# Optimization experiments

Measured on AMD Instinct MI355X. Metric: run time of the kernel, lower is better.

Reference implementation:

```python
import jax, jax.numpy as jnp
import numpy as np

DIM = 1024
N_HEADS = 16
DIM_FF = 4096
EPS = 1e-12


def layer_norm(x, gamma, beta):
    u = jnp.mean(x, axis=-1, keepdims=True)
    s = jnp.mean((x - u) ** 2, axis=-1, keepdims=True)
    return gamma * ((x - u) / jnp.sqrt(s + EPS)) + beta


def setup_inputs() -> dict:
    key = jax.random.key(0)
    ks = jax.random.split(key, 12)
    B, S, D, F = 2, 2048, DIM, DIM_FF
    init = lambda k, shape: (jax.random.normal(k, shape, dtype=jnp.float32) * 0.02)
    return {
        "x": jax.random.normal(ks[0], (B, S, D), dtype=jnp.float32),
        "mask": jnp.ones((B, S), dtype=jnp.int32),
        "wq": init(ks[1], (D, D)), "bq": jnp.zeros((D,), jnp.float32),
        "wk": init(ks[2], (D, D)), "bk": jnp.zeros((D,), jnp.float32),
        "wv": init(ks[3], (D, D)), "bv": jnp.zeros((D,), jnp.float32),
        "wo": init(ks[4], (D, D)), "bo": jnp.zeros((D,), jnp.float32),
        "g1": jnp.ones((D,), jnp.float32), "b1": jnp.zeros((D,), jnp.float32),
        "w1": init(ks[5], (D, F)), "bf1": jnp.zeros((F,), jnp.float32),
        "w2": init(ks[6], (F, D)), "bf2": jnp.zeros((D,), jnp.float32),
        "g2": jnp.ones((D,), jnp.float32), "b2": jnp.zeros((D,), jnp.float32),
    }


def reference(x, mask, wq, bq, wk, bk, wv, bv, wo, bo, g1, b1, w1, bf1, w2, bf2, g2, b2):
    B, S, D = x.shape
    H = N_HEADS
    W = D // H
    # QKV projections -> (B, H, S, W)
    def heads(y):
        return y.reshape(B, S, H, W).transpose(0, 2, 1, 3)
    q = heads(x @ wq + bq)
    k = heads(x @ wk + bk)
    v = heads(x @ wv + bv)
    # scaled dot-product attention with additive mask (exact module math)
    scores = jnp.einsum('bhsw,bhtw->bhst', q, k) / np.sqrt(W).astype(np.float32)
    m = mask.astype(jnp.float32)[:, None, None, :]  # (B,1,1,S)
    scores = scores - 10000.0 * (1.0 - m)
    attn = jax.nn.softmax(scores, axis=-1)
    h = jnp.einsum('bhst,bhtw->bhsw', attn, v).transpose(0, 2, 1, 3).reshape(B, S, D)
    # residual + LN1
    h = layer_norm(x + (h @ wo + bo), g1, b1)
    # position-wise FFN with exact-erf GELU, residual + LN2
    ff = jax.nn.gelu(h @ w1 + bf1, approximate=False) @ w2 + bf2
    return layer_norm(h + ff, g2, b2)
```

## Files before the change

kernel.cpp:

```cpp
#include <hip/hip_runtime.h>
#include <cstdint>
#include <cstddef>

using u16 = unsigned short;
using u32 = unsigned int;
using u64 = unsigned long long;

typedef __bf16 bf16x8 __attribute__((ext_vector_type(8)));
typedef float f32x4 __attribute__((ext_vector_type(4)));

static constexpr int Bb = 2, S = 2048, D = 1024, H = 16, W = 64, F = 4096;
static constexpr int M = Bb * S;

__device__ __forceinline__ float bf2f(u16 u) {
  union { u32 i; float f; } c; c.i = ((u32)u) << 16; return c.f;
}
__device__ __forceinline__ u16 f2bf(float f) {
  union { float f; u32 i; } c; c.f = f;
  u32 i = c.i;
  u32 r = (i + 0x7fffu + ((i >> 16) & 1u)) >> 16;
  return (u16)r;
}
__device__ __forceinline__ u16 f2bf_cvt(float f) {
  __bf16 b = (__bf16)f;
  union { __bf16 b; u16 u; } c; c.b = b; return c.u;
}
__device__ __forceinline__ __bf16 u2b(u16 x) {
  union { u16 u; __bf16 b; } c; c.u = x; return c.b;
}
__device__ __forceinline__ void stv(float* p, size_t i, float v) { p[i] = v; }
__device__ __forceinline__ void stv(u16* p, size_t i, float v)   { p[i] = f2bf(v); }
__device__ __forceinline__ float ldv(const float* p, size_t i) { return p[i]; }
__device__ __forceinline__ float ldv(const u16* p, size_t i)   { return bf2f(p[i]); }

__device__ __forceinline__ void async_cp16(const u16* g, u16* l) {
  __builtin_amdgcn_global_load_lds(
      (const __attribute__((address_space(1))) void*)g,
      (__attribute__((address_space(3))) void*)l, 16, 0, 0);
}

__device__ __forceinline__ void swizzle8(int& bx, int& by) {
  int bid = blockIdx.y * gridDim.x + blockIdx.x;
  int gpr = gridDim.x >> 3;
  int grp = bid >> 6, rem = bid & 63;
  int gm = grp / gpr, gn = grp - gm * gpr;
  by = gm * 8 + (rem >> 3);
  bx = gn * 8 + (rem & 7);
}

__global__ __launch_bounds__(256) void conv_x_kernel(
    const float* __restrict__ src, u16* __restrict__ dst)
{
  int i = (blockIdx.x * 256 + threadIdx.x) * 4;
  float4 v = *(const float4*)(src + i);
  u16 r[4] = { f2bf(v.x), f2bf(v.y), f2bf(v.z), f2bf(v.w) };
  *(uint2*)(dst + i) = *(const uint2*)r;
}

__global__ __launch_bounds__(256) void transpose_w_kernel(
    const float* __restrict__ src, u16* __restrict__ dst, int K, int N)
{
  __shared__ __align__(16) u16 T[64][72];
  const int tid = threadIdx.x;
  const int n0 = blockIdx.x * 64, k0 = blockIdx.y * 64;
#pragma unroll
  for (int t = 0; t < 4; t++) {
    int idx = tid + t * 256;
    int r = idx >> 4, c4 = (idx & 15) * 4;
    float4 v = *(const float4*)(src + (size_t)(k0 + r) * N + n0 + c4);
    T[c4 + 0][r] = f2bf(v.x); T[c4 + 1][r] = f2bf(v.y);
    T[c4 + 2][r] = f2bf(v.z); T[c4 + 3][r] = f2bf(v.w);
  }
  __syncthreads();
#pragma unroll
  for (int t = 0; t < 2; t++) {
    int idx = tid + t * 256;
    int r = idx >> 3, c8 = (idx & 7) * 8;
    *(uint4*)(dst + (size_t)(n0 + r) * K + k0 + c8) = *(const uint4*)(&T[r][c8]);
  }
}

template<int EPI, typename TC>
__global__ __launch_bounds__(256) void gemm_bt(
    const u16* __restrict__ A, const u16* __restrict__ BT,
    const float* __restrict__ bias, TC* __restrict__ C,
    int N, int K, float scale)
{
  __shared__ __align__(16) u16 As[2][128 * 32];
  __shared__ __align__(16) u16 Bs[2][128 * 32];
  const int tid = threadIdx.x;
  const int wave = tid >> 6, lane = tid & 63;
  const int quad = lane >> 4, l16 = lane & 15;
  int bx, by; swizzle8(bx, by);
  const int m0 = by * 128, n0 = bx * 128;
  const int wm = (wave >> 1) * 64, wn = (wave & 1) * 64;
  const int srow = lane >> 2;
  const int skoff = (lane & 3) * 8;

  f32x4 acc[4][4] = {};

  for (int k0 = 0; k0 < K; k0 += 64) {
#pragma unroll
    for (int h = 0; h < 2; h++) {
#pragma unroll
      for (int t = 0; t < 2; t++) {
        int slot = wave * 2 + t;
        int row = slot * 16 + srow;
        const u16* ga = A  + (size_t)(m0 + row) * K + k0 + h * 32 + skoff;
        const u16* gb = BT + (size_t)(n0 + row) * K + k0 + h * 32 + skoff;
        async_cp16(ga, As[h] + slot * 512);
        async_cp16(gb, Bs[h] + slot * 512);
      }
    }
    __syncthreads();

#pragma unroll
    for (int h = 0; h < 2; h++) {
      bf16x8 af[4], bfv[4];
#pragma unroll
      for (int i = 0; i < 4; i++)
        af[i] = *(const bf16x8*)(As[h] + (wm + i * 16 + l16) * 32 + quad * 8);
#pragma unroll
      for (int j = 0; j < 4; j++)
        bfv[j] = *(const bf16x8*)(Bs[h] + (wn + j * 16 + l16) * 32 + quad * 8);
#pragma unroll
      for (int i = 0; i < 4; i++)
#pragma unroll
        for (int j = 0; j < 4; j++)
          acc[i][j] = __builtin_amdgcn_mfma_f32_16x16x32_bf16(af[i], bfv[j], acc[i][j], 0, 0, 0);
    }
    __syncthreads();
  }

#pragma unroll
  for (int i = 0; i < 4; i++) {
#pragma unroll
    for (int j = 0; j < 4; j++) {
#pragma unroll
      for (int r = 0; r < 4; r++) {
        int row = m0 + wm + i * 16 + quad * 4 + r;
        int col = n0 + wn + j * 16 + l16;
        float val = acc[i][j][r] + bias[col];
        if (EPI == 2) {
          int sel = col >> 10, c = col & 1023;
          if (sel == 0) val *= scale;
          int bb = row >> 11, ss = row & 2047;
          int hh = c >> 6,  ww = c & 63;
          u16* dst = (u16*)C + (size_t)sel * M * D;
          dst[(((size_t)(bb * H + hh) * S) + ss) * W + ww] = f2bf(val);
        } else {
          stv(C, (size_t)row * N + col, val);
        }
      }
    }
  }
}

__global__ __launch_bounds__(512, 2) void gemm256_gelu(
    const u16* __restrict__ A, const u16* __restrict__ BT,
    const float* __restrict__ bias, u16* __restrict__ C)
{
  constexpr int GN = F, GK = D, NT = GK / 64;
  __shared__ __align__(16) u16 AL[2][2][128 * 64];
  __shared__ __align__(16) u16 BL[2][2][128 * 64];
  const int tid = threadIdx.x;
  const int wave = tid >> 6, lane = tid & 63;
  const int quad = lane >> 4, l16 = lane & 15;
  const int wm = wave >> 2, wn = wave & 3;
  int bx, by; swizzle8(bx, by);
  const int m0 = by * 256, n0 = bx * 256;
  const int lr = lane >> 3;
  const int kc8 = ((lane & 7) ^ lr) * 8;
  const int xb = (l16 & 7) * 16;
  const int brow0 = (wn & 1) * 64;
  const char* abase = (const char*)&AL[0][wm][0];
  const char* bbase = (const char*)&BL[0][wn >> 1][0];
  constexpr int BUFB = 2 * 128 * 64 * 2;

  f32x4 acc[8][4] = {};

  auto stA = [&](int t, int buf) {
#pragma unroll
    for (int half = 0; half < 2; half++)
#pragma unroll
      for (int j = 0; j < 2; j++) {
        const u16* g = A + (size_t)(m0 + half * 128 + (j * 8 + wave) * 8 + lr) * GK
                         + t * 64 + kc8;
        async_cp16(g, &AL[buf][half][(j * 8 + wave) * 512]);
      }
  };
  auto stB = [&](int t, int buf, int half) {
#pragma unroll
    for (int j = 0; j < 2; j++) {
      const u16* g = BT + (size_t)(n0 + half * 128 + (j * 8 + wave) * 8 + lr) * GK
                        + t * 64 + kc8;
      async_cp16(g, &BL[buf][half][(j * 8 + wave) * 512]);
    }
  };

  stA(0, 0);
  stB(0, 0, 0); stB(0, 0, 1);
  stB(1, 1, 0); stB(1, 1, 1);
  asm volatile("s_waitcnt vmcnt(4)" ::: "memory");
  __builtin_amdgcn_s_barrier();

  bf16x8 af[4][2], bf0[2][2], bf1v[2][2];

#pragma unroll 2
  for (int t = 0; t < NT; t++) {
    const int buf = t & 1;
    const char* ab = abase + buf * BUFB;
    const char* bb = bbase + buf * BUFB;

#pragma unroll
    for (int i = 0; i < 4; i++)
#pragma unroll
      for (int s = 0; s < 2; s++)
        af[i][s] = *(const bf16x8*)(ab + (i * 16 + l16) * 128 + (((s * 4 + quad) * 16) ^ xb));
#pragma unroll
    for (int j = 0; j < 2; j++)
#pragma unroll
      for (int s = 0; s < 2; s++)
        bf0[j][s] = *(const bf16x8*)(bb + (brow0 + j * 16 + l16) * 128 + (((s * 4 + quad) * 16) ^ xb));
    stA((t + 1) & (NT - 1), buf ^ 1);
    __builtin_amdgcn_s_barrier();
    __builtin_amdgcn_s_setprio(1);
#pragma unroll
    for (int i = 0; i < 4; i++)
#pragma unroll
      for (int j = 0; j < 2; j++)
#pragma unroll
        for (int s = 0; s < 2; s++)
          acc[i][j] = __builtin_amdgcn_mfma_f32_16x16x32_bf16(af[i][s], bf0[j][s], acc[i][j], 0, 0, 0);
    __builtin_amdgcn_s_setprio(0);
    __builtin_amdgcn_s_barrier();

#pragma unroll
    for (int j = 0; j < 2; j++)
#pragma unroll
      for (int s = 0; s < 2; s++)
        bf1v[j][s] = *(const bf16x8*)(bb + (brow0 + 32 + j * 16 + l16) * 128 + (((s * 4 + quad) * 16) ^ xb));
    __builtin_amdgcn_s_barrier();
    __builtin_amdgcn_s_setprio(1);
#pragma unroll
    for (int i = 0; i < 4; i++)
#pragma unroll
      for (int j = 0; j < 2; j++)
#pragma unroll
        for (int s = 0; s < 2; s++)
          acc[i][2 + j] = __builtin_amdgcn_mfma_f32_16x16x32_bf16(af[i][s], bf1v[j][s], acc[i][2 + j], 0, 0, 0);
    __builtin_amdgcn_s_setprio(0);
    __builtin_amdgcn_s_barrier();

#pragma unroll
    for (int i = 0; i < 4; i++)
#pragma unroll
      for (int s = 0; s < 2; s++)
        af[i][s] = *(const bf16x8*)(ab + (64 + i * 16 + l16) * 128 + (((s * 4 + quad) * 16) ^ xb));
    stB((t + 2) & (NT - 1), buf, 0);
    __builtin_amdgcn_s_barrier();
    __builtin_amdgcn_s_setprio(1);
#pragma unroll
    for (int i = 0; i < 4; i++)
#pragma unroll
      for (int j = 0; j < 2; j++)
#pragma unroll
        for (int s = 0; s < 2; s++)
          acc[4 + i][2 + j] = __builtin_amdgcn_mfma_f32_16x16x32_bf16(af[i][s], bf1v[j][s], acc[4 + i][2 + j], 0, 0, 0);
    __builtin_amdgcn_s_setprio(0);
    __builtin_amdgcn_s_barrier();

    stB((t + 2) & (NT - 1), buf, 1);
    __builtin_amdgcn_s_barrier();
    __builtin_amdgcn_s_setprio(1);
#pragma unroll
    for (int i = 0; i < 4; i++)
#pragma unroll
      for (int j = 0; j < 2; j++)
#pragma unroll
        for (int s = 0; s < 2; s++)
          acc[4 + i][j] = __builtin_amdgcn_mfma_f32_16x16x32_bf16(af[i][s], bf0[j][s], acc[4 + i][j], 0, 0, 0);
    __builtin_amdgcn_s_setprio(0);
    asm volatile("s_waitcnt vmcnt(4)" ::: "memory");
    __builtin_amdgcn_s_barrier();
  }

  asm volatile("s_waitcnt vmcnt(0)" ::: "memory");

#pragma unroll
  for (int i = 0; i < 8; i++) {
#pragma unroll
    for (int j = 0; j < 4; j++) {
#pragma unroll
      for (int r = 0; r < 4; r++) {
        int row = m0 + wm * 128 + i * 16 + quad * 4 + r;
        int col = n0 + wn * 64 + j * 16 + l16;
        float val = acc[i][j][r] + bias[col];
        val = 0.5f * val * (1.0f + erff(val * 0.70710678118654752f));
        C[(size_t)row * GN + col] = f2bf(val);
      }
    }
  }
}

template<typename TC>
__global__ __launch_bounds__(256) void gemm_bt_n64(
    const u16* __restrict__ A, const u16* __restrict__ BT,
    const float* __restrict__ bias, TC* __restrict__ C,
    int N, int K)
{
  __shared__ __align__(16) u16 As[2][128 * 32];
  __shared__ __align__(16) u16 Bs[2][64 * 32];
  const int tid = threadIdx.x;
  const int wave = tid >> 6, lane = tid & 63;
  const int quad = lane >> 4, l16 = lane & 15;
  int bx, by; swizzle8(bx, by);
  const int m0 = by * 128, n0 = bx * 64;
  const int wm = (wave >> 1) * 64, wn = (wave & 1) * 32;
  const int srow = lane >> 2;
  const int skoff = (lane & 3) * 8;

  f32x4 acc[4][2] = {};

  for (int k0 = 0; k0 < K; k0 += 64) {
#pragma unroll
    for (int h = 0; h < 2; h++) {
#pragma unroll
      for (int t = 0; t < 2; t++) {
        int slot = wave * 2 + t;
        int row = slot * 16 + srow;
        async_cp16(A + (size_t)(m0 + row) * K + k0 + h * 32 + skoff, As[h] + slot * 512);
      }
      int row = wave * 16 + srow;
      async_cp16(BT + (size_t)(n0 + row) * K + k0 + h * 32 + skoff, Bs[h] + wave * 512);
    }
    __syncthreads();

#pragma unroll
    for (int h = 0; h < 2; h++) {
      bf16x8 af[4], bfv[2];
#pragma unroll
      for (int i = 0; i < 4; i++)
        af[i] = *(const bf16x8*)(As[h] + (wm + i * 16 + l16) * 32 + quad * 8);
#pragma unroll
      for (int j = 0; j < 2; j++)
        bfv[j] = *(const bf16x8*)(Bs[h] + (wn + j * 16 + l16) * 32 + quad * 8);
#pragma unroll
      for (int i = 0; i < 4; i++)
#pragma unroll
        for (int j = 0; j < 2; j++)
          acc[i][j] = __builtin_amdgcn_mfma_f32_16x16x32_bf16(af[i], bfv[j], acc[i][j], 0, 0, 0);
    }
    __syncthreads();
  }

#pragma unroll
  for (int i = 0; i < 4; i++) {
#pragma unroll
    for (int j = 0; j < 2; j++) {
#pragma unroll
      for (int r = 0; r < 4; r++) {
        int row = m0 + wm + i * 16 + quad * 4 + r;
        int col = n0 + wn + j * 16 + l16;
        stv(C, (size_t)row * N + col, acc[i][j][r] + bias[col]);
      }
    }
  }
}

__global__ __launch_bounds__(256) void transpose_v_kernel(
    const u16* __restrict__ v, u16* __restrict__ vt)
{
  __shared__ __align__(16) u16 T[64][72];
  const int bh = blockIdx.y, k0 = blockIdx.x * 64, tid = threadIdx.x;
#pragma unroll
  for (int it = 0; it < 2; it++) {
    int vv = tid + it * 256;
    int key = vv >> 3, w0 = (vv & 7) * 8;
    union { uint4 q; u16 e[8]; } u;
    u.q = *(const uint4*)(v + ((size_t)bh * S + k0 + key) * W + w0);
#pragma unroll
    for (int j = 0; j < 8; j++) T[w0 + j][key] = u.e[j];
  }
  __syncthreads();
#pragma unroll
  for (int it = 0; it < 2; it++) {
    int vv = tid + it * 256;
    int w = vv >> 3, koff = (vv & 7) * 8;
    *(uint4*)(vt + ((size_t)bh * W + w) * S + k0 + koff) = *(const uint4*)(&T[w][koff]);
  }
}

__global__ __launch_bounds__(256) void fattn_kernel(
    const u16* __restrict__ q, const u16* __restrict__ k,
    const u16* __restrict__ vt, const int* __restrict__ mask,
    u16* __restrict__ o_parts, float* __restrict__ l_parts)
{
  __shared__ __align__(16) u16 QP[2][128][32];
  __shared__ __align__(16) u16 Kl[2][64][32];
  __shared__ __align__(16) u16 Vl[2][64][32];

  const int tid = threadIdx.x, wave = tid >> 6, lane = tid & 63;
  const int quad = lane >> 4, l16 = lane & 15;
  const int bh = blockIdx.y, b = bh >> 4, h = bh & 15;
  const int q0 = blockIdx.x * 128;
  const int half = blockIdx.z;
  const int kbase = half * (S / 2);
  const int wq0 = wave * 32;
  const int sr  = tid >> 3;
  const int sg  = tid & 7;
  const int sp  = sg >> 2;
  const int sc0 = sg * 8;
  const int ssw = (((sg & 3) ^ ((sr >> 1) & 3)) << 3);
  const int xr = (l16 >> 1) & 3;
  const int rq = ((quad ^ xr) << 3);

#pragma unroll
  for (int t = 0; t < 4; t++) {
    int row = sr + t * 32;
    *(uint4*)(&QP[sp][row][ssw]) =
        *(const uint4*)(q + ((size_t)bh * S + q0 + row) * W + sc0);
  }
  __syncthreads();
  bf16x8 aq[2][2];
#pragma unroll
  for (int g = 0; g < 2; g++)
#pragma unroll
    for (int kc = 0; kc < 2; kc++)
      aq[g][kc] = *(const bf16x8*)(&QP[kc][wq0 + g * 16 + l16][rq]);

  bf16x8 ones;
  {
    u16 ov = (l16 == 0) ? (u16)0x3F80 : (u16)0;
#pragma unroll
    for (int j = 0; j < 8; j++) ones[j] = u2b(ov);
  }

  f32x4 o_acc[2][4] = {};
  f32x4 l_acc[2] = {};

  uint4 kr0, kr1, vr0, vr1;
  int mv;
  kr0 = *(const uint4*)(k  + ((size_t)bh * S + kbase + sr     ) * W + sc0);
  kr1 = *(const uint4*)(k  + ((size_t)bh * S + kbase + sr + 32) * W + sc0);
  vr0 = *(const uint4*)(vt + ((size_t)bh * W + sr     ) * S + kbase + sc0);
  vr1 = *(const uint4*)(vt + ((size_t)bh * W + sr + 32) * S + kbase + sc0);
  mv  = mask[b * S + kbase + lane];

  constexpr int NT = S / 128;
  for (int kt = 0; kt < NT; kt++) {
    __syncthreads();
    *(uint4*)(&Kl[sp][sr     ][ssw]) = kr0;
    *(uint4*)(&Kl[sp][sr + 32][ssw]) = kr1;
    *(uint4*)(&Vl[sp][sr     ][ssw]) = vr0;
    *(uint4*)(&Vl[sp][sr + 32][ssw]) = vr1;
    u64 km = __ballot(mv != 0);
    __syncthreads();

    if (kt + 1 < NT) {
      int kn = kbase + (kt + 1) * 64;
      kr0 = *(const uint4*)(k  + ((size_t)bh * S + kn + sr     ) * W + sc0);
      kr1 = *(const uint4*)(k  + ((size_t)bh * S + kn + sr + 32) * W + sc0);
      vr0 = *(const uint4*)(vt + ((size_t)bh * W + sr     ) * S + kn + sc0);
      vr1 = *(const uint4*)(vt + ((size_t)bh * W + sr + 32) * S + kn + sc0);
      mv  = mask[b * S + kn + lane];
    }

#pragma unroll
    for (int tn = 0; tn < 4; tn++) {
      bf16x8 bk0 = *(const bf16x8*)(&Kl[0][tn * 16 + l16][rq]);
      bf16x8 bk1 = *(const bf16x8*)(&Kl[1][tn * 16 + l16][rq]);
      u32 nib = (u32)(km >> (tn * 16 + quad * 4)) & 0xFu;
      int slotp = (((tn & 1) * 2 + (quad >> 1)) ^ xr) * 8 + (quad & 1) * 4;
#pragma unroll
      for (int g = 0; g < 2; g++) {
        f32x4 s4 = {};
        s4 = __builtin_amdgcn_mfma_f32_16x16x32_bf16(bk0, aq[g][0], s4, 0, 0, 0);
        s4 = __builtin_amdgcn_mfma_f32_16x16x32_bf16(bk1, aq[g][1], s4, 0, 0, 0);
        union { u64 u; u16 e[4]; } pw;
#pragma unroll
        for (int r = 0; r < 4; r++) {
          float pm = (float)((nib >> r) & 1u);
          pw.e[r] = f2bf_cvt(__expf(s4[r]) * pm);
        }
        *(u64*)(&QP[tn >> 1][wq0 + g * 16 + l16][slotp]) = pw.u;
      }
    }

#pragma unroll
    for (int kc = 0; kc < 2; kc++) {
      bf16x8 ap0 = *(const bf16x8*)(&QP[kc][wq0      + l16][rq]);
      bf16x8 ap1 = *(const bf16x8*)(&QP[kc][wq0 + 16 + l16][rq]);
#pragma unroll
      for (int tn = 0; tn < 4; tn++) {
        bf16x8 bv = *(const bf16x8*)(&Vl[kc][tn * 16 + l16][rq]);
        o_acc[0][tn] = __builtin_amdgcn_mfma_f32_16x16x32_bf16(ap0, bv, o_acc[0][tn], 0, 0, 0);
        o_acc[1][tn] = __builtin_amdgcn_mfma_f32_16x16x32_bf16(ap1, bv, o_acc[1][tn], 0, 0, 0);
      }
      l_acc[0] = __builtin_amdgcn_mfma_f32_16x16x32_bf16(ap0, ones, l_acc[0], 0, 0, 0);
      l_acc[1] = __builtin_amdgcn_mfma_f32_16x16x32_bf16(ap1, ones, l_acc[1], 0, 0, 0);
    }
  }

  u16* ob = o_parts + (size_t)half * M * D;
  float* lb = l_parts + (size_t)half * M * H;
#pragma unroll
  for (int g = 0; g < 2; g++) {
#pragma unroll
    for (int r = 0; r < 4; r++) {
      float lsum = __shfl(l_acc[g][r], lane & 0x30);
      int sg2 = q0 + wq0 + g * 16 + quad * 4 + r;
      if (l16 == 0) lb[((size_t)b * S + sg2) * H + h] = lsum;
#pragma unroll
      for (int tn = 0; tn < 4; tn++) {
        ob[((size_t)b * S + sg2) * D + h * W + tn * 16 + l16] = f2bf_cvt(o_acc[g][tn][r]);
      }
    }
  }
}

__global__ __launch_bounds__(256) void combine_attn(
    const u16* __restrict__ o_parts, const float* __restrict__ l_parts,
    u16* __restrict__ attn)
{
  size_t idx = ((size_t)blockIdx.x * 256 + threadIdx.x) * 8;
  int row = (int)(idx >> 10);
  int h = ((int)idx >> 6) & 15;
  float l = l_parts[(size_t)row * H + h] + l_parts[(size_t)M * H + (size_t)row * H + h];
  float inv = 1.0f / l;
  union { uint4 v; u16 e[8]; } a, bq, o;
  a.v  = *(const uint4*)(o_parts + idx);
  bq.v = *(const uint4*)(o_parts + (size_t)M * D + idx);
#pragma unroll
  for (int j = 0; j < 8; j++)
    o.e[j] = f2bf((bf2f(a.e[j]) + bf2f(bq.e[j])) * inv);
  *(uint4*)(attn + idx) = o.v;
}

template<typename TA, typename TR, typename TO>
__global__ __launch_bounds__(256) void ln_res_kernel(
    const TA* __restrict__ a, const TR* __restrict__ r,
    const float* __restrict__ g, const float* __restrict__ be,
    TO* __restrict__ out)
{
  const int tid = threadIdx.x, lane = tid & 63;
  const int row = blockIdx.x * 4 + (tid >> 6);
  const TA* ap = a + (size_t)row * D;
  const TR* rp = r + (size_t)row * D;
  float hv[16];
  float s = 0.f;
#pragma unroll
  for (int c = 0; c < 16; c++) {
    int d = c * 64 + lane;
    hv[c] = ldv(ap, d) + ldv(rp, d);
    s += hv[c];
  }
#pragma unroll
  for (int d = 1; d < 64; d <<= 1) s += __shfl_xor(s, d);
  float mean = s * (1.0f / D);
  float v = 0.f;
#pragma unroll
  for (int c = 0; c < 16; c++) { float t = hv[c] - mean; v += t * t; }
#pragma unroll
  for (int d = 1; d < 64; d <<= 1) v += __shfl_xor(v, d);
  float inv = rsqrtf(v * (1.0f / D) + 1e-12f);
#pragma unroll
  for (int c = 0; c < 16; c++) {
    int d = c * 64 + lane;
    stv(out, (size_t)row * D + d, g[d] * ((hv[c] - mean) * inv) + be[d]);
  }
}

extern "C" void kernel_launch(void* const* d_in, const int* in_sizes, int n_in,
                              void* d_out, int out_size, void* d_ws, size_t ws_size,
                              hipStream_t stream)
{
  const float* x  = (const float*)d_in[0];
  const int* mask = (const int*)d_in[1];
  const float* wq = (const float*)d_in[2];  const float* bq  = (const float*)d_in[3];
  const float* wk = (const float*)d_in[4];  const float* bk  = (const float*)d_in[5];
  const float* wv = (const float*)d_in[6];  const float* bv  = (const float*)d_in[7];
  const float* wo = (const float*)d_in[8];  const float* bo  = (const float*)d_in[9];
  const float* g1 = (const float*)d_in[10]; const float* b1  = (const float*)d_in[11];
  const float* w1 = (const float*)d_in[12]; const float* bf1 = (const float*)d_in[13];
  const float* w2 = (const float*)d_in[14]; const float* bf2 = (const float*)d_in[15];
  const float* g2 = (const float*)d_in[16]; const float* b2  = (const float*)d_in[17];

  char* ws = (char*)d_ws;
  const size_t MB = 1024 * 1024;
  u16* wqkvT = (u16*)(ws + 0 * MB);
  u16* woT   = (u16*)(ws + 6 * MB);
  u16* w1T   = (u16*)(ws + 0 * MB);
  u16* w2T   = (u16*)(ws + 0 * MB);
  u16* xb    = (u16*)(ws + 8 * MB);
  u16* vt    = (u16*)(ws + 8 * MB);
  u16* q     = (u16*)(ws + 16 * MB);
  u16* proj  = (u16*)(ws + 16 * MB);
  u16* kb    = (u16*)(ws + 24 * MB);
  u16* vb    = (u16*)(ws + 32 * MB);
  u16* oparts = (u16*)(ws + 32 * MB);
  float* lparts = (float*)(ws + 0 * MB);
  u16* attn  = (u16*)(ws + 32 * MB);
  u16* ff1   = (u16*)(ws + 8 * MB);
  float* bqkv = (float*)(ws + 40 * MB);
  u16* h1    = (u16*)(ws + 40 * MB);
  float* out = (float*)d_out;

  dim3 blk(256);

  conv_x_kernel<<<dim3(M * D / 1024), blk, 0, stream>>>(x, xb);
  transpose_w_kernel<<<dim3(16, 16), blk, 0, stream>>>(wq, wqkvT,            D, D);
  transpose_w_kernel<<<dim3(16, 16), blk, 0, stream>>>(wk, wqkvT + 1024*1024, D, D);
  transpose_w_kernel<<<dim3(16, 16), blk, 0, stream>>>(wv, wqkvT + 2048*1024, D, D);
  transpose_w_kernel<<<dim3(16, 16), blk, 0, stream>>>(wo, woT,              D, D);
  hipMemcpyAsync(bqkv,        bq, D * sizeof(float), hipMemcpyDeviceToDevice, stream);
  hipMemcpyAsync(bqkv + 1024, bk, D * sizeof(float), hipMemcpyDeviceToDevice, stream);
  hipMemcpyAsync(bqkv + 2048, bv, D * sizeof(float), hipMemcpyDeviceToDevice, stream);

  gemm_bt<2, u16><<<dim3(3072 / 128, M / 128), blk, 0, stream>>>(
      xb, wqkvT, bqkv, q, 3072, D, 0.125f);

  transpose_v_kernel<<<dim3(S / 64, Bb * H), blk, 0, stream>>>(vb, vt);
  fattn_kernel<<<dim3(S / 128, Bb * H, 2), blk, 0, stream>>>(
      q, kb, vt, mask, oparts, lparts);
  combine_attn<<<dim3(M * D / 2048), blk, 0, stream>>>(oparts, lparts, attn);

  gemm_bt_n64<u16><<<dim3(D / 64, M / 128), blk, 0, stream>>>(
      attn, woT, bo, proj, D, D);
  ln_res_kernel<float, u16, u16><<<dim3(M / 4), blk, 0, stream>>>(x, proj, g1, b1, h1);

  transpose_w_kernel<<<dim3(F / 64, D / 64), blk, 0, stream>>>(w1, w1T, D, F);
  gemm256_gelu<<<dim3(F / 256, M / 256), dim3(512), 0, stream>>>(
      h1, w1T, bf1, ff1);

  transpose_w_kernel<<<dim3(D / 64, F / 64), blk, 0, stream>>>(w2, w2T, F, D);
  gemm_bt_n64<float><<<dim3(D / 64, M / 128), blk, 0, stream>>>(
      ff1, w2T, bf2, out, D, F);
  ln_res_kernel<u16, float, float><<<dim3(M / 4), blk, 0, stream>>>(h1, out, g2, b2, out);
}
```

Before: 401.9 us.

## Use split-K 256x128 tiled GEMM for FFN2 with fused three-way LN reduction

Replaces the FFN down-projection GEMM (128x64 tiles, K=4096) with a 512-thread, 256x128-tile kernel that splits K in two across blockIdx.z and writes two fp32 partial outputs. A new LayerNorm kernel sums the residual, both partials and the bias before normalising. The goal is better data reuse per tile and more blocks to fill the GPU despite the larger tiles. The cost is an extra fp32 partial buffer written and read, and the path needs at least 64 MB of workspace, otherwise the old path runs.

```diff
diff --git a/kernel.cpp b/kernel.cpp
--- a/kernel.cpp
+++ b/kernel.cpp
@@ -303,6 +303,152 @@
   }
 }
 
+__global__ __launch_bounds__(512, 2) void gemm_ffn2_splitk(
+    const u16* __restrict__ A, const u16* __restrict__ BT,
+    float* __restrict__ P0, float* __restrict__ P1)
+{
+  constexpr int GK = F, NT = 32;
+  __shared__ __align__(16) u16 AL[2][2][128 * 64];
+  __shared__ __align__(16) u16 BL[2][128 * 64];
+  const int tid = threadIdx.x;
+  const int wave = tid >> 6, lane = tid & 63;
+  const int quad = lane >> 4, l16 = lane & 15;
+  const int wm = wave >> 1, wn = wave & 1;
+  int bx, by; swizzle8(bx, by);
+  const int m0 = by * 256, n0 = bx * 128;
+  const int kbase = blockIdx.z * (F / 2);
+  const int lr = lane >> 3;
+  const int kc8 = ((lane & 7) ^ lr) * 8;
+  const int xb = (l16 & 7) * 16;
+  const int arow0 = (wm & 1) * 64;
+  const int brow0 = wn * 64;
+  const char* abase = (const char*)&AL[0][wm >> 1][0];
+  const char* bbase = (const char*)&BL[0][0];
+  constexpr int ABUF = 2 * 128 * 64 * 2;
+  constexpr int BBUF = 128 * 64 * 2;
+
+  f32x4 acc[4][4] = {};
+
+  auto stA2 = [&](int t, int buf, int rp) {
+#pragma unroll
+    for (int rr = 0; rr < 2; rr++) {
+      int rd = rp * 2 + rr;
+      const u16* g = A + (size_t)(m0 + rd * 64 + wave * 8 + lr) * GK
+                       + kbase + t * 64 + kc8;
+      async_cp16(g, &AL[buf][rd >> 1][((rd & 1) * 8 + wave) * 512]);
+    }
+  };
+  auto stB1 = [&](int t, int buf, int rd) {
+    const u16* g = BT + (size_t)(n0 + rd * 64 + wave * 8 + lr) * GK
+                      + kbase + t * 64 + kc8;
+    async_cp16(g, &BL[buf][(rd * 8 + wave) * 512]);
+  };
+
+  stA2(0, 0, 0); stA2(0, 0, 1);
+  stB1(0, 0, 0); stB1(0, 0, 1);
+  stB1(1, 1, 0); stB1(1, 1, 1);
+  asm volatile("s_waitcnt vmcnt(2)" ::: "memory");
+  __builtin_amdgcn_s_barrier();
+
+  bf16x8 af[2][2], bf0[2][2], bf1v[2][2];
+
+#pragma unroll 2
+  for (int t = 0; t < NT; t++) {
+    const int buf = t & 1;
+    const char* ab = abase + buf * ABUF;
+    const char* bb = bbase + buf * BBUF;
+
+#pragma unroll
+    for (int i = 0; i < 2; i++)
+#pragma unroll
+      for (int s = 0; s < 2; s++)
+        af[i][s] = *(const bf16x8*)(ab + (arow0 + i * 16 + l16) * 128 + (((s * 4 + quad) * 16) ^ xb));
+#pragma unroll
+    for (int j = 0; j < 2; j++)
+#pragma unroll
+      for (int s = 0; s < 2; s++)
+        bf0[j][s] = *(const bf16x8*)(bb + (brow0 + j * 16 + l16) * 128 + (((s * 4 + quad) * 16) ^ xb));
+    stA2((t + 1) & (NT - 1), buf ^ 1, 0);
+    __builtin_amdgcn_s_barrier();
+    __builtin_amdgcn_s_setprio(1);
+#pragma unroll
+    for (int i = 0; i < 2; i++)
+#pragma unroll
+      for (int j = 0; j < 2; j++)
+#pragma unroll
+        for (int s = 0; s < 2; s++)
+          acc[i][j] = __builtin_amdgcn_mfma_f32_16x16x32_bf16(af[i][s], bf0[j][s], acc[i][j], 0, 0, 0);
+    __builtin_amdgcn_s_setprio(0);
+    __builtin_amdgcn_s_barrier();
+
+#pragma unroll
+    for (int j = 0; j < 2; j++)
+#pragma unroll
+      for (int s = 0; s < 2; s++)
+        bf1v[j][s] = *(const bf16x8*)(bb + (brow0 + 32 + j * 16 + l16) * 128 + (((s * 4 + quad) * 16) ^ xb));
+    stA2((t + 1) & (NT - 1), buf ^ 1, 1);
+    __builtin_amdgcn_s_barrier();
+    __builtin_amdgcn_s_setprio(1);
+#pragma unroll
+    for (int i = 0; i < 2; i++)
+#pragma unroll
+      for (int j = 0; j < 2; j++)
+#pragma unroll
+        for (int s = 0; s < 2; s++)
+          acc[i][2 + j] = __builtin_amdgcn_mfma_f32_16x16x32_bf16(af[i][s], bf1v[j][s], acc[i][2 + j], 0, 0, 0);
+    __builtin_amdgcn_s_setprio(0);
+    __builtin_amdgcn_s_barrier();
+
+#pragma unroll
+    for (int i = 0; i < 2; i++)
+#pragma unroll
+      for (int s = 0; s < 2; s++)
+        af[i][s] = *(const bf16x8*)(ab + (arow0 + 32 + i * 16 + l16) * 128 + (((s * 4 + quad) * 16) ^ xb));
+    stB1((t + 2) & (NT - 1), buf, 0);
+    __builtin_amdgcn_s_barrier();
+    __builtin_amdgcn_s_setprio(1);
+#pragma unroll
+    for (int i = 0; i < 2; i++)
+#pragma unroll
+      for (int j = 0; j < 2; j++)
+#pragma unroll
+        for (int s = 0; s < 2; s++)
+          acc[2 + i][2 + j] = __builtin_amdgcn_mfma_f32_16x16x32_bf16(af[i][s], bf1v[j][s], acc[2 + i][2 + j], 0, 0, 0);
+    __builtin_amdgcn_s_setprio(0);
+    __builtin_amdgcn_s_barrier();
+
+    stB1((t + 2) & (NT - 1), buf, 1);
+    __builtin_amdgcn_s_barrier();
+    __builtin_amdgcn_s_setprio(1);
+#pragma unroll
+    for (int i = 0; i < 2; i++)
+#pragma unroll
+      for (int j = 0; j < 2; j++)
+#pragma unroll
+        for (int s = 0; s < 2; s++)
+          acc[2 + i][j] = __builtin_amdgcn_mfma_f32_16x16x32_bf16(af[i][s], bf0[j][s], acc[2 + i][j], 0, 0, 0);
+    __builtin_amdgcn_s_setprio(0);
+    asm volatile("s_waitcnt vmcnt(2)" ::: "memory");
+    __builtin_amdgcn_s_barrier();
+  }
+
+  asm volatile("s_waitcnt vmcnt(0)" ::: "memory");
+
+  float* P = blockIdx.z ? P1 : P0;
+#pragma unroll
+  for (int i = 0; i < 4; i++) {
+#pragma unroll
+    for (int j = 0; j < 4; j++) {
+#pragma unroll
+      for (int r = 0; r < 4; r++) {
+        int row = m0 + wm * 64 + i * 16 + quad * 4 + r;
+        int col = n0 + wn * 64 + j * 16 + l16;
+        P[(size_t)row * D + col] = acc[i][j][r];
+      }
+    }
+  }
+}
+
 template<typename TC>
 __global__ __launch_bounds__(256) void gemm_bt_n64(
     const u16* __restrict__ A, const u16* __restrict__ BT,
@@ -568,6 +714,41 @@
   for (int c = 0; c < 16; c++) {
     int d = c * 64 + lane;
     stv(out, (size_t)row * D + d, g[d] * ((hv[c] - mean) * inv) + be[d]);
+  }
+}
+
+__global__ __launch_bounds__(256) void ln_res3_kernel(
+    const u16* __restrict__ a, const float* __restrict__ p0,
+    const float* __restrict__ p1, const float* __restrict__ bias,
+    const float* __restrict__ g, const float* __restrict__ be,
+    float* __restrict__ out)
+{
+  const int tid = threadIdx.x, lane = tid & 63;
+  const int row = blockIdx.x * 4 + (tid >> 6);
+  const u16* ap = a + (size_t)row * D;
+  const float* q0 = p0 + (size_t)row * D;
+  const float* q1 = p1 + (size_t)row * D;
+  float hv[16];
+  float s = 0.f;
+#pragma unroll
+  for (int c = 0; c < 16; c++) {
+    int d = c * 64 + lane;
+    hv[c] = bf2f(ap[d]) + q0[d] + q1[d] + bias[d];
+    s += hv[c];
+  }
+#pragma unroll
+  for (int d = 1; d < 64; d <<= 1) s += __shfl_xor(s, d);
+  float mean = s * (1.0f / D);
+  float v = 0.f;
+#pragma unroll
+  for (int c = 0; c < 16; c++) { float t = hv[c] - mean; v += t * t; }
+#pragma unroll
+  for (int d = 1; d < 64; d <<= 1) v += __shfl_xor(v, d);
+  float inv = rsqrtf(v * (1.0f / D) + 1e-12f);
+#pragma unroll
+  for (int c = 0; c < 16; c++) {
+    int d = c * 64 + lane;
+    out[(size_t)row * D + d] = g[d] * ((hv[c] - mean) * inv) + be[d];
   }
 }
 
@@ -604,7 +785,10 @@
   u16* ff1   = (u16*)(ws + 8 * MB);
   float* bqkv = (float*)(ws + 40 * MB);
   u16* h1    = (u16*)(ws + 40 * MB);
+  float* part1 = (float*)(ws + 48 * MB);
   float* out = (float*)d_out;
+
+  const bool bigws = ws_size >= (size_t)64 * MB;
 
   dim3 blk(256);
 
@@ -634,7 +818,13 @@
       h1, w1T, bf1, ff1);
 
   transpose_w_kernel<<<dim3(D / 64, F / 64), blk, 0, stream>>>(w2, w2T, F, D);
-  gemm_bt_n64<float><<<dim3(D / 64, M / 128), blk, 0, stream>>>(
-      ff1, w2T, bf2, out, D, F);
-  ln_res_kernel<u16, float, float><<<dim3(M / 4), blk, 0, stream>>>(h1, out, g2, b2, out);
-}
+  if (bigws) {
+    gemm_ffn2_splitk<<<dim3(D / 128, M / 256, 2), dim3(512), 0, stream>>>(
+        ff1, w2T, out, part1);
+    ln_res3_kernel<<<dim3(M / 4), blk, 0, stream>>>(h1, out, part1, bf2, g2, b2, out);
+  } else {
+    gemm_bt_n64<float><<<dim3(D / 64, M / 128), blk, 0, stream>>>(
+        ff1, w2T, bf2, out, D, F);
+    ln_res_kernel<u16, float, float><<<dim3(M / 4), blk, 0, stream>>>(h1, out, g2, b2, out);
+  }
+}
```

Result: no change. 401.2 us (-0.2%).
